# Kernel tuning notes

Measured on AMD Instinct MI355X. Metric: run time of the kernel, lower is better.

Reference implementation:

```python
import jax, jax.numpy as jnp
import numpy as np

N_NODES = 100000
N_EDGES = 1600000
IN_DIM = 128
OUT_DIM = 128


def setup_inputs() -> dict:
    key = jax.random.key(0)
    ks = jax.random.split(key, 8)
    x = jax.random.normal(ks[0], (N_NODES, IN_DIM), dtype=jnp.float32)
    one_hot_h = jax.random.normal(ks[1], (N_NODES, OUT_DIM), dtype=jnp.float32)
    # three candidate-op linear transforms (in_dim -> out_dim)
    W0 = jax.random.normal(ks[2], (IN_DIM, OUT_DIM), dtype=jnp.float32) * 0.05
    W1 = jax.random.normal(ks[3], (IN_DIM, OUT_DIM), dtype=jnp.float32) * 0.05
    W2 = jax.random.normal(ks[4], (IN_DIM, OUT_DIM), dtype=jnp.float32) * 0.05
    # sparse mask_matrix in COO form: out[r] += v * H[c]
    mask_rows = jax.random.randint(ks[5], (N_EDGES,), 0, N_NODES, dtype=jnp.int32)
    mask_cols = jax.random.randint(ks[6], (N_EDGES,), 0, N_NODES, dtype=jnp.int32)
    mask_vals = jax.random.uniform(ks[7], (N_EDGES,), dtype=jnp.float32)
    return {"x": x, "one_hot_h": one_hot_h, "W0": W0, "W1": W1, "W2": W2,
            "mask_rows": mask_rows, "mask_cols": mask_cols, "mask_vals": mask_vals}


def reference(x, one_hot_h, W0, W1, W2, mask_rows, mask_cols, mask_vals):
    # Original: sum_k spmm(mask_matrix, op_k(x)) + spmm(mask_matrix, one_hot_h).
    # spmm is linear, so summing per-op outputs pre-aggregation is exact and
    # fuses K spmm launches into one sparse aggregation pass.
    H = x @ W0 + x @ W1 + x @ W2 + one_hot_h              # [N, out_dim]
    gathered = mask_vals[:, None] * H[mask_cols]          # [E, out_dim]
    out = jax.ops.segment_sum(gathered, mask_rows, num_segments=x.shape[0])
    return out
```

## Files before the change

### kernel.cpp

```cpp
#include <hip/hip_runtime.h>
#include <hip/hip_bf16.h>

#define N_NODES 100000
#define N_EDGES 1600000
#define DIM 128

#define NBIN 256
#define RPP  391
#define PCAP 8192
#define P1_BLOCKS 256
#define CHUNK (N_EDGES / P1_BLOCKS)

typedef unsigned int uint_t;
typedef unsigned short ushort_t;
typedef float f32x4 __attribute__((ext_vector_type(4)));
typedef __bf16 bf16x8 __attribute__((ext_vector_type(8)));

__device__ inline ushort_t f2bf(float f) {
    uint_t u = __float_as_uint(f);
    uint_t r = (u + 0x7FFFu + ((u >> 16) & 1u)) >> 16;
    return (ushort_t)r;
}
__device__ inline float bf2f(uint_t lo16) { return __uint_as_float(lo16 << 16); }

__global__ __launch_bounds__(256) void pass1_bin(
        const int* __restrict__ rows, const int* __restrict__ cols,
        const float* __restrict__ vals, int* __restrict__ psize,
        long long* __restrict__ slab,
        const float* __restrict__ W0, const float* __restrict__ W1,
        const float* __restrict__ W2, ushort_t* __restrict__ WT) {
    if (blockIdx.x >= P1_BLOCKS) {
        int i = (blockIdx.x - P1_BLOCKS) * 256 + threadIdx.x;
        if (i < DIM * DIM) {
            int m = i & 127, k = i >> 7;
            float s = W0[k * DIM + m] + W1[k * DIM + m] + W2[k * DIM + m];
            WT[m * DIM + k] = f2bf(s);
        }
        return;
    }
    __shared__ int hist[NBIN];
    __shared__ int binoff[NBIN];
    __shared__ int resv[NBIN];
    __shared__ int curs[NBIN];
    __shared__ long long ebuf[CHUNK];
    __shared__ int edest[CHUNK];

    int t = threadIdx.x;
    int e0 = blockIdx.x * CHUNK;

    if (t < NBIN) hist[t] = 0;
    __syncthreads();

    for (int i = t; i < CHUNK; i += 256) {
        int r = rows[e0 + i];
        atomicAdd(&hist[r / RPP], 1);
    }
    __syncthreads();

    if (t < 64) {
        int b = t * 4;
        int v0 = hist[b], v1 = hist[b + 1], v2 = hist[b + 2], v3 = hist[b + 3];
        int s = v0 + v1 + v2 + v3;
        int incl = s;
#pragma unroll
        for (int d = 1; d < 64; d <<= 1) {
            int o = __shfl_up(incl, d, 64);
            if (t >= d) incl += o;
        }
        int excl = incl - s;
        binoff[b]     = excl;
        binoff[b + 1] = excl + v0;
        binoff[b + 2] = excl + v0 + v1;
        binoff[b + 3] = excl + v0 + v1 + v2;
    }
    __syncthreads();

    if (t < NBIN) {
        int len = hist[t];
        int r = (len > 0) ? atomicAdd(&psize[t], len) : 0;
        resv[t] = t * PCAP + r;
        curs[t] = binoff[t];
    }
    __syncthreads();

    for (int i = t; i < CHUNK; i += 256) {
        int   r = rows[e0 + i];
        int   c = cols[e0 + i];
        float v = vals[e0 + i];
        int b  = r / RPP;
        int lr = r - b * RPP;
        int pos = atomicAdd(&curs[b], 1);
        uint_t key = ((uint_t)lr << 17) | (uint_t)c;
        ebuf[pos]  = ((long long)__float_as_int(v) << 32) | (long long)key;
        edest[pos] = resv[b] + (pos - binoff[b]);
    }
    __syncthreads();

    for (int i = t; i < CHUNK; i += 256)
        slab[edest[i]] = ebuf[i];
}

__global__ void pscan(const int* __restrict__ psize, int* __restrict__ pbase,
                      int* __restrict__ off) {
    int lane = threadIdx.x & 63;
    int b = lane * 4;
    int v0 = min(psize[b], PCAP),     v1 = min(psize[b + 1], PCAP);
    int v2 = min(psize[b + 2], PCAP), v3 = min(psize[b + 3], PCAP);
    int s = v0 + v1 + v2 + v3;
    int incl = s;
#pragma unroll
    for (int d = 1; d < 64; d <<= 1) {
        int o = __shfl_up(incl, d, 64);
        if (lane >= d) incl += o;
    }
    int excl = incl - s;
    pbase[b]     = excl;
    pbase[b + 1] = excl + v0;
    pbase[b + 2] = excl + v0 + v1;
    pbase[b + 3] = excl + v0 + v1 + v2;
    if (lane == 0) off[N_NODES] = N_EDGES;
}

__global__ __launch_bounds__(256) void pass2_sort(
        const long long* __restrict__ slab, const int* __restrict__ psize,
        const int* __restrict__ pbase, int* __restrict__ off,
        long long* __restrict__ csr) {
    __shared__ int cnt[RPP + 1];
    __shared__ int loff[RPP + 1];
    __shared__ int curs[RPP];
    __shared__ long long ebuf[PCAP];

    int p = blockIdx.x, t = threadIdx.x;
    int n = min(psize[p], PCAP);
    int base = pbase[p];
    int rlo = p * RPP;
    int nrows = N_NODES - rlo; if (nrows > RPP) nrows = RPP;
    const long long* seg = slab + (long long)p * PCAP;

    for (int i = t; i < RPP + 1; i += 256) cnt[i] = 0;
    __syncthreads();

    for (int i = t; i < n; i += 256) {
        uint_t key = (uint_t)(seg[i] & 0xFFFFFFFFll);
        atomicAdd(&cnt[key >> 17], 1);
    }
    __syncthreads();

    if (t < 64) {
        int b7 = t * 7;
        int v[7]; int s = 0;
#pragma unroll
        for (int k = 0; k < 7; ++k) {
            int idx = b7 + k;
            v[k] = (idx < RPP) ? cnt[idx] : 0;
            s += v[k];
        }
        int incl = s;
#pragma unroll
        for (int d = 1; d < 64; d <<= 1) {
            int o = __shfl_up(incl, d, 64);
            if (t >= d) incl += o;
        }
        int run = incl - s;
#pragma unroll
        for (int k = 0; k < 7; ++k) {
            int idx = b7 + k;
            if (idx < RPP) loff[idx] = run;
            run += v[k];
        }
    }
    __syncthreads();

    for (int i = t; i < nrows; i += 256) {
        curs[i] = loff[i];
        off[rlo + i] = base + loff[i];
    }
    __syncthreads();

    for (int i = t; i < n; i += 256) {
        long long ev = seg[i];
        uint_t key = (uint_t)(ev & 0xFFFFFFFFll);
        int lr = key >> 17;
        uint_t c = key & 0x1FFFFu;
        int pos = atomicAdd(&curs[lr], 1);
        ebuf[pos] = (long long)(((unsigned long long)ev & 0xFFFFFFFF00000000ull) | c);
    }
    __syncthreads();

    for (int i = t; i < n; i += 256)
        __builtin_nontemporal_store(ebuf[i], &csr[base + i]);
}

__global__ __launch_bounds__(256) void gemm_mfma(const float* __restrict__ x,
                                                 const float* __restrict__ oh,
                                                 const ushort_t* __restrict__ WT,
                                                 uint_t* __restrict__ H16) {
    int tid = threadIdx.x;
    int wv = tid >> 6, l = tid & 63;
    int lr = l & 15, kg = l >> 4;
    int hr = blockIdx.x * 64 + wv * 16 + lr;
    int hr_c = (hr < N_NODES) ? hr : (N_NODES - 1);

    f32x4 acc[8] = {};
    const float* xrow = x + (size_t)hr_c * DIM;

#pragma unroll
    for (int s = 0; s < 4; ++s) {
        float4 xa = *(const float4*)(xrow + s * 32 + kg * 8);
        float4 xb = *(const float4*)(xrow + s * 32 + kg * 8 + 4);
        union { bf16x8 v; __bf16 h[8]; } b;
        b.h[0] = (__bf16)xa.x; b.h[1] = (__bf16)xa.y;
        b.h[2] = (__bf16)xa.z; b.h[3] = (__bf16)xa.w;
        b.h[4] = (__bf16)xb.x; b.h[5] = (__bf16)xb.y;
        b.h[6] = (__bf16)xb.z; b.h[7] = (__bf16)xb.w;
#pragma unroll
        for (int mt = 0; mt < 8; ++mt) {
            bf16x8 a = *(const bf16x8*)&WT[(mt * 16 + lr) * DIM + s * 32 + kg * 8];
            acc[mt] = __builtin_amdgcn_mfma_f32_16x16x32_bf16(a, b.v, acc[mt], 0, 0, 0);
        }
    }

    if (hr < N_NODES) {
#pragma unroll
        for (int mt = 0; mt < 8; ++mt) {
            int c0 = mt * 16 + kg * 4;
            float4 o = *(const float4*)&oh[(size_t)hr * DIM + c0];
            float f0 = acc[mt].x + o.x, f1 = acc[mt].y + o.y;
            float f2 = acc[mt].z + o.z, f3 = acc[mt].w + o.w;
            uint2 pk;
            pk.x = (uint_t)f2bf(f0) | ((uint_t)f2bf(f1) << 16);
            pk.y = (uint_t)f2bf(f2) | ((uint_t)f2bf(f3) << 16);
            *(uint2*)&H16[(size_t)hr * (DIM / 2) + c0 / 2] = pk;
        }
    }
}

__global__ __launch_bounds__(256) void gather_kernel(const uint_t* __restrict__ H16,
                                                     const int* __restrict__ off,
                                                     const long long* __restrict__ csr,
                                                     float* __restrict__ out) {
    int tid  = threadIdx.x;
    int wave = tid >> 6;
    int lane = tid & 63;
    int grp  = lane >> 4;
    int il   = lane & 15;
    int wid  = blockIdx.x * 16 + wave * 4 + grp;

    int s = off[wid], e = off[wid + 1];
    float acc[8] = {0.f, 0.f, 0.f, 0.f, 0.f, 0.f, 0.f, 0.f};

    int p = s;
    for (; p + 3 < e; p += 4) {
        long long cv0 = __builtin_nontemporal_load(&csr[p]);
        long long cv1 = __builtin_nontemporal_load(&csr[p + 1]);
        long long cv2 = __builtin_nontemporal_load(&csr[p + 2]);
        long long cv3 = __builtin_nontemporal_load(&csr[p + 3]);
        uint4 h0 = *(const uint4*)&H16[(long long)(int)(cv0 & 0x1FFFF) * (DIM / 2) + il * 4];
        uint4 h1 = *(const uint4*)&H16[(long long)(int)(cv1 & 0x1FFFF) * (DIM / 2) + il * 4];
        uint4 h2 = *(const uint4*)&H16[(long long)(int)(cv2 & 0x1FFFF) * (DIM / 2) + il * 4];
        uint4 h3 = *(const uint4*)&H16[(long long)(int)(cv3 & 0x1FFFF) * (DIM / 2) + il * 4];
        float v0 = __int_as_float((int)(cv0 >> 32));
        float v1 = __int_as_float((int)(cv1 >> 32));
        float v2 = __int_as_float((int)(cv2 >> 32));
        float v3 = __int_as_float((int)(cv3 >> 32));
#define ACC8(h, v)                                                        \
        acc[0] += (v) * bf2f((h).x & 0xFFFFu); acc[1] += (v) * bf2f((h).x >> 16); \
        acc[2] += (v) * bf2f((h).y & 0xFFFFu); acc[3] += (v) * bf2f((h).y >> 16); \
        acc[4] += (v) * bf2f((h).z & 0xFFFFu); acc[5] += (v) * bf2f((h).z >> 16); \
        acc[6] += (v) * bf2f((h).w & 0xFFFFu); acc[7] += (v) * bf2f((h).w >> 16);
        ACC8(h0, v0) ACC8(h1, v1) ACC8(h2, v2) ACC8(h3, v3)
    }
    for (; p < e; ++p) {
        long long cv = __builtin_nontemporal_load(&csr[p]);
        float v = __int_as_float((int)(cv >> 32));
        uint4 h = *(const uint4*)&H16[(long long)(int)(cv & 0x1FFFF) * (DIM / 2) + il * 4];
        ACC8(h, v)
    }
#undef ACC8

    float* op = &out[(long long)wid * DIM + il * 8];
    f32x4 o0 = {acc[0], acc[1], acc[2], acc[3]};
    f32x4 o1 = {acc[4], acc[5], acc[6], acc[7]};
    __builtin_nontemporal_store(o0, (f32x4*)op);
    __builtin_nontemporal_store(o1, (f32x4*)(op + 4));
}

extern "C" void kernel_launch(void* const* d_in, const int* in_sizes, int n_in,
                              void* d_out, int out_size, void* d_ws, size_t ws_size,
                              hipStream_t stream) {
    const float* x    = (const float*)d_in[0];
    const float* oh   = (const float*)d_in[1];
    const float* W0   = (const float*)d_in[2];
    const float* W1   = (const float*)d_in[3];
    const float* W2   = (const float*)d_in[4];
    const int*   rows = (const int*)d_in[5];
    const int*   cols = (const int*)d_in[6];
    const float* vals = (const float*)d_in[7];
    float* out = (float*)d_out;

    char* p = (char*)d_ws;
    size_t oW    = 0;
    size_t oH    = oW + 64 * 1024;
    size_t oOff  = oH + (size_t)N_NODES * DIM * 2;
    size_t oPs   = oOff + (size_t)(N_NODES + 32) * 4;
    size_t oPb   = oPs + 2048;
    size_t oSlab = oPb + 2048;
    size_t oCsr  = oSlab + (size_t)NBIN * PCAP * 8;

    ushort_t*  WT    = (ushort_t*)(p + oW);
    uint_t*    H16   = (uint_t*)(p + oH);
    int*       off   = (int*)(p + oOff);
    int*       psize = (int*)(p + oPs);
    int*       pbase = (int*)(p + oPb);
    long long* slab  = (long long*)(p + oSlab);
    long long* csr   = (long long*)(p + oCsr);

    (void)hipMemsetAsync(psize, 0, NBIN * sizeof(int), stream);
    pass1_bin<<<P1_BLOCKS + 64, 256, 0, stream>>>(rows, cols, vals, psize, slab,
                                                  W0, W1, W2, WT);
    pscan<<<1, 64, 0, stream>>>(psize, pbase, off);
    gemm_mfma<<<(N_NODES + 63) / 64, 256, 0, stream>>>(x, oh, WT, H16);
    pass2_sort<<<NBIN, 256, 0, stream>>>(slab, psize, pbase, off, csr);
    gather_kernel<<<N_NODES / 16, 256, 0, stream>>>(H16, off, csr, out);
}
```

Before: 164.9 us.

## Fold scan into sort kernel, stage GEMM inputs via LDS, double binning blocks

The separate one-block prefix-scan launch is removed and every pass2_sort block recomputes the bin base offsets redundantly in shared memory. The GEMM now loads x and one_hot_h with coalesced nontemporal loads, converts them to bf16 into an LDS tile and reads MFMA operands from there, replacing strided per-lane global loads. The binning pass uses twice as many blocks with half-size chunks, and pass2_sort is launched before the GEMM. The cost is redundant scan work in each block and rounding one_hot_h to bf16 before it is added, which is an extra precision loss.

```diff
diff --git a/kernel.cpp b/kernel.cpp
--- a/kernel.cpp
+++ b/kernel.cpp
@@ -8,7 +8,7 @@
 #define NBIN 256
 #define RPP  391
 #define PCAP 8192
-#define P1_BLOCKS 256
+#define P1_BLOCKS 512
 #define CHUNK (N_EDGES / P1_BLOCKS)
 
 typedef unsigned int uint_t;
@@ -16,10 +16,9 @@
 typedef float f32x4 __attribute__((ext_vector_type(4)));
 typedef __bf16 bf16x8 __attribute__((ext_vector_type(8)));
 
-__device__ inline ushort_t f2bf(float f) {
+__device__ inline uint_t f2bf(float f) {
     uint_t u = __float_as_uint(f);
-    uint_t r = (u + 0x7FFFu + ((u >> 16) & 1u)) >> 16;
-    return (ushort_t)r;
+    return (u + 0x7FFFu + ((u >> 16) & 1u)) >> 16;
 }
 __device__ inline float bf2f(uint_t lo16) { return __uint_as_float(lo16 << 16); }
 
@@ -34,7 +33,7 @@
         if (i < DIM * DIM) {
             int m = i & 127, k = i >> 7;
             float s = W0[k * DIM + m] + W1[k * DIM + m] + W2[k * DIM + m];
-            WT[m * DIM + k] = f2bf(s);
+            WT[m * DIM + k] = (ushort_t)f2bf(s);
         }
         return;
     }
@@ -100,45 +99,45 @@
         slab[edest[i]] = ebuf[i];
 }
 
-__global__ void pscan(const int* __restrict__ psize, int* __restrict__ pbase,
-                      int* __restrict__ off) {
-    int lane = threadIdx.x & 63;
-    int b = lane * 4;
-    int v0 = min(psize[b], PCAP),     v1 = min(psize[b + 1], PCAP);
-    int v2 = min(psize[b + 2], PCAP), v3 = min(psize[b + 3], PCAP);
-    int s = v0 + v1 + v2 + v3;
-    int incl = s;
-#pragma unroll
-    for (int d = 1; d < 64; d <<= 1) {
-        int o = __shfl_up(incl, d, 64);
-        if (lane >= d) incl += o;
-    }
-    int excl = incl - s;
-    pbase[b]     = excl;
-    pbase[b + 1] = excl + v0;
-    pbase[b + 2] = excl + v0 + v1;
-    pbase[b + 3] = excl + v0 + v1 + v2;
-    if (lane == 0) off[N_NODES] = N_EDGES;
-}
-
 __global__ __launch_bounds__(256) void pass2_sort(
         const long long* __restrict__ slab, const int* __restrict__ psize,
-        const int* __restrict__ pbase, int* __restrict__ off,
-        long long* __restrict__ csr) {
+        int* __restrict__ off, long long* __restrict__ csr) {
+    __shared__ int pb[NBIN + 1];
     __shared__ int cnt[RPP + 1];
     __shared__ int loff[RPP + 1];
     __shared__ int curs[RPP];
     __shared__ long long ebuf[PCAP];
 
     int p = blockIdx.x, t = threadIdx.x;
+
+    if (t < 64) {
+        int b = t * 4;
+        int v0 = min(psize[b], PCAP),     v1 = min(psize[b + 1], PCAP);
+        int v2 = min(psize[b + 2], PCAP), v3 = min(psize[b + 3], PCAP);
+        int s = v0 + v1 + v2 + v3;
+        int incl = s;
+#pragma unroll
+        for (int d = 1; d < 64; d <<= 1) {
+            int o = __shfl_up(incl, d, 64);
+            if (t >= d) incl += o;
+        }
+        int excl = incl - s;
+        pb[b]     = excl;
+        pb[b + 1] = excl + v0;
+        pb[b + 2] = excl + v0 + v1;
+        pb[b + 3] = excl + v0 + v1 + v2;
+        if (t == 63) pb[NBIN] = incl;
+    }
+    for (int i = t; i < RPP + 1; i += 256) cnt[i] = 0;
+    __syncthreads();
+
     int n = min(psize[p], PCAP);
-    int base = pbase[p];
+    int base = pb[p];
     int rlo = p * RPP;
     int nrows = N_NODES - rlo; if (nrows > RPP) nrows = RPP;
     const long long* seg = slab + (long long)p * PCAP;
 
-    for (int i = t; i < RPP + 1; i += 256) cnt[i] = 0;
-    __syncthreads();
+    if (p == NBIN - 1 && t == 0) off[N_NODES] = pb[NBIN];
 
     for (int i = t; i < n; i += 256) {
         uint_t key = (uint_t)(seg[i] & 0xFFFFFFFFll);
@@ -191,45 +190,71 @@
         __builtin_nontemporal_store(ebuf[i], &csr[base + i]);
 }
 
+#define GROWS 64
+#define XSTR 136
 __global__ __launch_bounds__(256) void gemm_mfma(const float* __restrict__ x,
                                                  const float* __restrict__ oh,
                                                  const ushort_t* __restrict__ WT,
                                                  uint_t* __restrict__ H16) {
+    __shared__ ushort_t xs[GROWS * XSTR];
     int tid = threadIdx.x;
     int wv = tid >> 6, l = tid & 63;
     int lr = l & 15, kg = l >> 4;
-    int hr = blockIdx.x * 64 + wv * 16 + lr;
-    int hr_c = (hr < N_NODES) ? hr : (N_NODES - 1);
+    int lrow = wv * 16 + lr;
+    long long base_row = (long long)blockIdx.x * GROWS;
+    long long hr = base_row + lrow;
+
+    const f32x4* xg = (const f32x4*)x;
+#pragma unroll
+    for (int i = 0; i < 8; ++i) {
+        int g = tid + i * 256;
+        int row = g >> 5, c4 = g & 31;
+        long long sr = base_row + row; if (sr >= N_NODES) sr = N_NODES - 1;
+        f32x4 v = __builtin_nontemporal_load(xg + sr * 32 + c4);
+        ushort_t* d = &xs[row * XSTR + c4 * 4];
+        d[0] = (ushort_t)f2bf(v.x); d[1] = (ushort_t)f2bf(v.y);
+        d[2] = (ushort_t)f2bf(v.z); d[3] = (ushort_t)f2bf(v.w);
+    }
+    __syncthreads();
 
     f32x4 acc[8] = {};
-    const float* xrow = x + (size_t)hr_c * DIM;
-
 #pragma unroll
     for (int s = 0; s < 4; ++s) {
-        float4 xa = *(const float4*)(xrow + s * 32 + kg * 8);
-        float4 xb = *(const float4*)(xrow + s * 32 + kg * 8 + 4);
-        union { bf16x8 v; __bf16 h[8]; } b;
-        b.h[0] = (__bf16)xa.x; b.h[1] = (__bf16)xa.y;
-        b.h[2] = (__bf16)xa.z; b.h[3] = (__bf16)xa.w;
-        b.h[4] = (__bf16)xb.x; b.h[5] = (__bf16)xb.y;
-        b.h[6] = (__bf16)xb.z; b.h[7] = (__bf16)xb.w;
+        bf16x8 b = *(const bf16x8*)&xs[lrow * XSTR + s * 32 + kg * 8];
 #pragma unroll
         for (int mt = 0; mt < 8; ++mt) {
             bf16x8 a = *(const bf16x8*)&WT[(mt * 16 + lr) * DIM + s * 32 + kg * 8];
-            acc[mt] = __builtin_amdgcn_mfma_f32_16x16x32_bf16(a, b.v, acc[mt], 0, 0, 0);
-        }
-    }
+            acc[mt] = __builtin_amdgcn_mfma_f32_16x16x32_bf16(a, b, acc[mt], 0, 0, 0);
+        }
+    }
+    __syncthreads();
+
+    const f32x4* og = (const f32x4*)oh;
+#pragma unroll
+    for (int i = 0; i < 8; ++i) {
+        int g = tid + i * 256;
+        int row = g >> 5, c4 = g & 31;
+        long long sr = base_row + row; if (sr >= N_NODES) sr = N_NODES - 1;
+        f32x4 v = __builtin_nontemporal_load(og + sr * 32 + c4);
+        ushort_t* d = &xs[row * XSTR + c4 * 4];
+        d[0] = (ushort_t)f2bf(v.x); d[1] = (ushort_t)f2bf(v.y);
+        d[2] = (ushort_t)f2bf(v.z); d[3] = (ushort_t)f2bf(v.w);
+    }
+    __syncthreads();
 
     if (hr < N_NODES) {
 #pragma unroll
         for (int mt = 0; mt < 8; ++mt) {
             int c0 = mt * 16 + kg * 4;
-            float4 o = *(const float4*)&oh[(size_t)hr * DIM + c0];
-            float f0 = acc[mt].x + o.x, f1 = acc[mt].y + o.y;
-            float f2 = acc[mt].z + o.z, f3 = acc[mt].w + o.w;
+            const uint_t* ow = (const uint_t*)&xs[lrow * XSTR + c0];
+            uint_t w0 = ow[0], w1 = ow[1];
+            float f0 = acc[mt].x + bf2f(w0 & 0xFFFFu);
+            float f1 = acc[mt].y + bf2f(w0 >> 16);
+            float f2 = acc[mt].z + bf2f(w1 & 0xFFFFu);
+            float f3 = acc[mt].w + bf2f(w1 >> 16);
             uint2 pk;
-            pk.x = (uint_t)f2bf(f0) | ((uint_t)f2bf(f1) << 16);
-            pk.y = (uint_t)f2bf(f2) | ((uint_t)f2bf(f3) << 16);
+            pk.x = f2bf(f0) | (f2bf(f1) << 16);
+            pk.y = f2bf(f2) | (f2bf(f3) << 16);
             *(uint2*)&H16[(size_t)hr * (DIM / 2) + c0 / 2] = pk;
         }
     }
@@ -247,7 +272,13 @@
     int wid  = blockIdx.x * 16 + wave * 4 + grp;
 
     int s = off[wid], e = off[wid + 1];
-    float acc[8] = {0.f, 0.f, 0.f, 0.f, 0.f, 0.f, 0.f, 0.f};
+    float acc[8] = {};
+
+#define ACC8(h, v)                                                            \
+    acc[0] += (v) * bf2f((h).x & 0xFFFFu); acc[1] += (v) * bf2f((h).x >> 16); \
+    acc[2] += (v) * bf2f((h).y & 0xFFFFu); acc[3] += (v) * bf2f((h).y >> 16); \
+    acc[4] += (v) * bf2f((h).z & 0xFFFFu); acc[5] += (v) * bf2f((h).z >> 16); \
+    acc[6] += (v) * bf2f((h).w & 0xFFFFu); acc[7] += (v) * bf2f((h).w >> 16);
 
     int p = s;
     for (; p + 3 < e; p += 4) {
@@ -263,11 +294,6 @@
         float v1 = __int_as_float((int)(cv1 >> 32));
         float v2 = __int_as_float((int)(cv2 >> 32));
         float v3 = __int_as_float((int)(cv3 >> 32));
-#define ACC8(h, v)                                                        \
-        acc[0] += (v) * bf2f((h).x & 0xFFFFu); acc[1] += (v) * bf2f((h).x >> 16); \
-        acc[2] += (v) * bf2f((h).y & 0xFFFFu); acc[3] += (v) * bf2f((h).y >> 16); \
-        acc[4] += (v) * bf2f((h).z & 0xFFFFu); acc[5] += (v) * bf2f((h).z >> 16); \
-        acc[6] += (v) * bf2f((h).w & 0xFFFFu); acc[7] += (v) * bf2f((h).w >> 16);
         ACC8(h0, v0) ACC8(h1, v1) ACC8(h2, v2) ACC8(h3, v3)
     }
     for (; p < e; ++p) {
@@ -303,23 +329,20 @@
     size_t oH    = oW + 64 * 1024;
     size_t oOff  = oH + (size_t)N_NODES * DIM * 2;
     size_t oPs   = oOff + (size_t)(N_NODES + 32) * 4;
-    size_t oPb   = oPs + 2048;
-    size_t oSlab = oPb + 2048;
+    size_t oSlab = oPs + 4096;
     size_t oCsr  = oSlab + (size_t)NBIN * PCAP * 8;
 
     ushort_t*  WT    = (ushort_t*)(p + oW);
     uint_t*    H16   = (uint_t*)(p + oH);
     int*       off   = (int*)(p + oOff);
     int*       psize = (int*)(p + oPs);
-    int*       pbase = (int*)(p + oPb);
     long long* slab  = (long long*)(p + oSlab);
     long long* csr   = (long long*)(p + oCsr);
 
     (void)hipMemsetAsync(psize, 0, NBIN * sizeof(int), stream);
     pass1_bin<<<P1_BLOCKS + 64, 256, 0, stream>>>(rows, cols, vals, psize, slab,
                                                   W0, W1, W2, WT);
-    pscan<<<1, 64, 0, stream>>>(psize, pbase, off);
-    gemm_mfma<<<(N_NODES + 63) / 64, 256, 0, stream>>>(x, oh, WT, H16);
-    pass2_sort<<<NBIN, 256, 0, stream>>>(slab, psize, pbase, off, csr);
+    pass2_sort<<<NBIN, 256, 0, stream>>>(slab, psize, off, csr);
+    gemm_mfma<<<(N_NODES + GROWS - 1) / GROWS, 256, 0, stream>>>(x, oh, WT, H16);
     gather_kernel<<<N_NODES / 16, 256, 0, stream>>>(H16, off, csr, out);
 }
```

Measured after the change: 162.9 us. About the same (-1.2%).
